# Kernel optimization log

Measured on AMD Instinct MI355X. Metric: run time of the kernel, lower is better.

Reference implementation:

```python
import jax, jax.numpy as jnp
import numpy as np

SAMPLE_RATE = 16000
N_TRANSIENTS = 20
TRANSIENT_SAMPLES = 1600  # int(0.1 s * 16000 Hz)
BATCH = 64
MAX_TRANSIENTS = 256
AUDIO_LEN = 160000  # 10 s @ 16 kHz


def setup_inputs() -> dict:
    key = jax.random.key(0)
    k1, k2, k3, k4 = jax.random.split(key, 4)
    # timings in seconds, sorted per batch (as in generate_random_transients)
    transient_timings = jnp.sort(
        jax.random.uniform(k1, (BATCH, MAX_TRANSIENTS), dtype=jnp.float32) * 9.0, axis=1)
    transient_ids = jax.random.randint(k2, (BATCH, MAX_TRANSIENTS), 0, N_TRANSIENTS)
    transient_gains = 0.1 + 0.9 * jax.random.uniform(k3, (BATCH, MAX_TRANSIENTS), dtype=jnp.float32)
    transient_templates = jax.random.normal(k4, (N_TRANSIENTS, TRANSIENT_SAMPLES), dtype=jnp.float32)
    return {
        "transient_timings": transient_timings,
        "transient_ids": transient_ids,
        "transient_gains": transient_gains,
        "transient_templates": transient_templates,
        "audio_length": AUDIO_LEN,
    }


def reference(transient_timings, transient_ids, transient_gains, transient_templates, audio_length):
    n_tr, L = transient_templates.shape
    # start sample of each transient (timings are non-negative, so floor == int())
    t_sample = jnp.floor(transient_timings * SAMPLE_RATE).astype(jnp.int32)  # [B, T]
    # skip conditions from the original loop: gain <= 0, id >= n_transients, start >= audio_length
    valid = (transient_gains > 0) & (transient_ids < n_tr) & (t_sample < audio_length)
    # gather templates: [B, T, L]
    tmpl = transient_templates[jnp.clip(transient_ids, 0, n_tr - 1)]
    vals = tmpl * (transient_gains * valid.astype(transient_gains.dtype))[..., None]
    # destination positions: [B, T, L]; positions >= audio_length are dropped (truncation)
    pos = t_sample[..., None] + jnp.arange(L, dtype=jnp.int32)

    def scatter_one(p, v):
        # p, v: [T, L] -> scatter-add into [audio_length]
        return jnp.zeros((audio_length,), v.dtype).at[p.reshape(-1)].add(
            v.reshape(-1), mode='drop')

    return jax.vmap(scatter_one)(pos, vals)  # [B, audio_length]
```

## Files before the change

kernel.cpp:

```cpp
#include <hip/hip_runtime.h>


constexpr int SR    = 16000;
constexpr int TL    = 1600;
constexpr int MAXT  = 256;
constexpr int NTHR  = 256;
constexpr int CHUNK = 1024;
constexpr int PAD   = 1024;
constexpr int ROWP  = PAD + TL + PAD;

__global__ __launch_bounds__(256)
void pad_templates(const float* __restrict__ templates, float* __restrict__ tpad, int n_tr)
{
    const int total = n_tr * ROWP;
    for (int i = blockIdx.x * blockDim.x + threadIdx.x; i < total;
         i += gridDim.x * blockDim.x) {
        const int r = i / ROWP;
        const int t = (i - r * ROWP) - PAD;
        tpad[i] = ((unsigned)t < (unsigned)TL) ? templates[r * TL + t] : 0.0f;
    }
}

__global__ __launch_bounds__(NTHR)
void transient_gather(const float* __restrict__ timings,
                      const int*   __restrict__ ids,
                      const float* __restrict__ gains,
                      const float* __restrict__ tpad,
                      float*       __restrict__ out,
                      int T, int n_tr, int A)
{
    __shared__ int2               s_m[MAXT];
    __shared__ unsigned long long s_mask[NTHR / 64];

    const int b      = blockIdx.y;
    const int chunk0 = blockIdx.x * CHUNK;
    const int tid    = (int)threadIdx.x;

    {
        const float tm = timings[(size_t)b * T + tid];
        const float g  = gains  [(size_t)b * T + tid];
        const int   id = ids    [(size_t)b * T + tid];
        const int   ts = (int)floorf(tm * (float)SR);
        const bool ok  = (g > 0.0f) & (id < n_tr) & (ts < A);
        const int tsc  = min(max(ts, 0), A);
        const int idc  = min(max(id, 0), n_tr - 1);
        s_m[tid] = make_int2((tsc << 8) | idc, ok ? __float_as_int(g) : 0);
        const bool ov = (tsc < chunk0 + CHUNK) && (tsc + TL > chunk0);
        const unsigned long long mball = __ballot(ov);
        if ((tid & 63) == 0) s_mask[tid >> 6] = mball;
    }
    __syncthreads();

    int lo = T, hi = -1;
#pragma unroll
    for (int w = 0; w < NTHR / 64; ++w) {
        const unsigned long long mw = s_mask[w];
        if (mw) {
            lo = min(lo, w * 64 + (int)__builtin_ctzll(mw));
            hi = max(hi, w * 64 + 63 - (int)__builtin_clzll(mw));
        }
    }

    float acc[4] = {0.f, 0.f, 0.f, 0.f};

    for (int j = lo; j <= hi; ++j) {
        const int2 mj = s_m[j];
        const int  mx  = __builtin_amdgcn_readfirstlane(mj.x);
        const int  mgb = __builtin_amdgcn_readfirstlane(mj.y);
        if (mgb == 0) continue;
        const float g  = __int_as_float(mgb);
        const int   ts = mx >> 8;
        const float* __restrict__ p =
            tpad + (size_t)(mx & 255) * ROWP + PAD + (chunk0 - ts);
#pragma unroll
        for (int k = 0; k < 4; ++k)
            acc[k] = fmaf(g, p[tid + k * NTHR], acc[k]);
    }

    float* ob = out + (size_t)b * A + chunk0 + tid;
#pragma unroll
    for (int k = 0; k < 4; ++k) {
        if (chunk0 + tid + k * NTHR < A)
            __builtin_nontemporal_store(acc[k], &ob[k * NTHR]);
    }
}

__global__ __launch_bounds__(NTHR)
void transient_gather_guard(const float* __restrict__ timings, const int* __restrict__ ids,
                            const float* __restrict__ gains, const float* __restrict__ templates,
                            float* __restrict__ out, int T, int n_tr, int A)
{
    __shared__ int2               s_m[MAXT];
    __shared__ unsigned long long s_mask[NTHR / 64];
    const int b = blockIdx.y, chunk0 = blockIdx.x * CHUNK, tid = (int)threadIdx.x;
    {
        const float tm = timings[(size_t)b * T + tid];
        const float g  = gains  [(size_t)b * T + tid];
        const int   id = ids    [(size_t)b * T + tid];
        const int   ts = (int)floorf(tm * (float)SR);
        const bool ok  = (g > 0.0f) & (id < n_tr) & (ts < A);
        const int tsc  = min(max(ts, 0), A);
        const int idc  = min(max(id, 0), n_tr - 1);
        s_m[tid] = make_int2((tsc << 8) | idc, ok ? __float_as_int(g) : 0);
        const bool ov = (tsc < chunk0 + CHUNK) && (tsc + TL > chunk0);
        const unsigned long long mball = __ballot(ov);
        if ((tid & 63) == 0) s_mask[tid >> 6] = mball;
    }
    __syncthreads();
    int lo = T, hi = -1;
#pragma unroll
    for (int w = 0; w < NTHR / 64; ++w) {
        const unsigned long long mw = s_mask[w];
        if (mw) {
            lo = min(lo, w * 64 + (int)__builtin_ctzll(mw));
            hi = max(hi, w * 64 + 63 - (int)__builtin_clzll(mw));
        }
    }
    float acc[4] = {0.f, 0.f, 0.f, 0.f};
    const int off_base = chunk0 + tid;
    for (int j = lo; j <= hi; ++j) {
        const int2 m = s_m[j];
        const int ts = m.x >> 8;
        const float g = __int_as_float(m.y);
        const float* __restrict__ row = templates + (size_t)(m.x & 255) * TL;
        const int off0 = off_base - ts;
#pragma unroll
        for (int k = 0; k < 4; ++k) {
            const int o = off0 + k * NTHR;
            if ((unsigned)o < (unsigned)TL) acc[k] += g * row[o];
        }
    }
    float* ob = out + (size_t)b * A + off_base;
#pragma unroll
    for (int k = 0; k < 4; ++k)
        if (off_base + k * NTHR < A) __builtin_nontemporal_store(acc[k], &ob[k * NTHR]);
}

extern "C" void kernel_launch(void* const* d_in, const int* in_sizes, int n_in,
                              void* d_out, int out_size, void* d_ws, size_t ws_size,
                              hipStream_t stream) {
    const float* timings   = (const float*)d_in[0];
    const int*   ids       = (const int*)  d_in[1];
    const float* gains     = (const float*)d_in[2];
    const float* templates = (const float*)d_in[3];
    float*       out       = (float*)d_out;

    const int T    = MAXT;
    const int B    = in_sizes[0] / T;
    const int n_tr = in_sizes[3] / TL;
    const int A    = out_size / B;

    dim3 grid((A + CHUNK - 1) / CHUNK, B), block(NTHR);
    const size_t need = (size_t)n_tr * ROWP * sizeof(float);
    if (ws_size >= need) {
        float* tpad = (float*)d_ws;
        pad_templates<<<dim3(80), dim3(256), 0, stream>>>(templates, tpad, n_tr);
        transient_gather<<<grid, block, 0, stream>>>(timings, ids, gains, tpad, out,
                                                     T, n_tr, A);
    } else {
        transient_gather_guard<<<grid, block, 0, stream>>>(timings, ids, gains, templates,
                                                           out, T, n_tr, A);
    }
}
```

Before: 25.06 us.

## Stage all templates in LDS and compute per-wave sub-chunks in one kernel

Replaces the pad-templates pre-kernel plus the global-memory gather with a single kernel that copies all 20 templates (128 KB) into shared memory. Each block handles a quarter of one batch row, and each wave processes 1024-sample sub-chunks with 16 accumulators per lane and per-wave ballot overlap detection. This removes the extra launch and the global or L2 template reads. In exchange it uses far fewer blocks (256 blocks of 1024 threads), each doing a large LDS fill per block, and adds clamped, predicated loads.

```diff
diff --git a/kernel.cpp b/kernel.cpp
--- a/kernel.cpp
+++ b/kernel.cpp
@@ -4,38 +4,114 @@
 constexpr int SR    = 16000;
 constexpr int TL    = 1600;
 constexpr int MAXT  = 256;
-constexpr int NTHR  = 256;
-constexpr int CHUNK = 1024;
-constexpr int PAD   = 1024;
-constexpr int ROWP  = PAD + TL + PAD;
+constexpr int NTR   = 20;
+constexpr int NTHR  = 1024;
+constexpr int SUB   = 1024;
+constexpr int KPL   = 16;
+constexpr int QUART = 4;
 
-__global__ __launch_bounds__(256)
-void pad_templates(const float* __restrict__ templates, float* __restrict__ tpad, int n_tr)
+__global__ __launch_bounds__(NTHR)
+void transient_lds(const float* __restrict__ timings,
+                   const int*   __restrict__ ids,
+                   const float* __restrict__ gains,
+                   const float* __restrict__ templates,
+                   float*       __restrict__ out,
+                   int T, int n_tr, int A)
 {
-    const int total = n_tr * ROWP;
-    for (int i = blockIdx.x * blockDim.x + threadIdx.x; i < total;
-         i += gridDim.x * blockDim.x) {
-        const int r = i / ROWP;
-        const int t = (i - r * ROWP) - PAD;
-        tpad[i] = ((unsigned)t < (unsigned)TL) ? templates[r * TL + t] : 0.0f;
+    __shared__ float s_tmpl[NTR * TL];
+    __shared__ int2  s_m[MAXT];
+
+    const int b    = blockIdx.x / QUART;
+    const int q    = blockIdx.x - b * QUART;
+    const int tid  = (int)threadIdx.x;
+    const int lane = tid & 63;
+    const int wave = tid >> 6;
+
+    const int qlen = (A + QUART - 1) / QUART;
+    const int q0   = q * qlen;
+    const int qend = min(A, q0 + qlen);
+
+    {
+        const float4* src = reinterpret_cast<const float4*>(templates);
+        float4*       dst = reinterpret_cast<float4*>(s_tmpl);
+        const int nv = (n_tr * TL) / 4;
+        for (int i = tid; i < nv; i += NTHR) dst[i] = src[i];
+    }
+    if (tid < T) {
+        const float tm = timings[(size_t)b * T + tid];
+        const float g  = gains  [(size_t)b * T + tid];
+        const int   id = ids    [(size_t)b * T + tid];
+        const int   ts = (int)floorf(tm * (float)SR);
+        const bool ok  = (g > 0.0f) & (id < n_tr) & (ts < A);
+        const int tsc  = min(max(ts, 0), A);
+        const int idc  = min(max(id, 0), n_tr - 1);
+        s_m[tid] = make_int2((tsc << 8) | idc, ok ? __float_as_int(g) : 0);
+    }
+    __syncthreads();
+
+    int tsr[4];
+#pragma unroll
+    for (int qq = 0; qq < 4; ++qq) tsr[qq] = s_m[qq * 64 + lane].x >> 8;
+
+    const int nsub = (qend - q0 + SUB - 1) / SUB;
+
+    for (int sc = wave; sc < nsub; sc += NTHR / 64) {
+        const int sub0 = q0 + sc * SUB;
+
+        int lo = T, hi = -1;
+#pragma unroll
+        for (int qq = 0; qq < 4; ++qq) {
+            const bool ov = (tsr[qq] < sub0 + SUB) & (tsr[qq] + TL > sub0);
+            const unsigned long long m = __ballot(ov);
+            if (m) {
+                lo = min(lo, qq * 64 + (int)__builtin_ctzll(m));
+                hi = max(hi, qq * 64 + 63 - (int)__builtin_clzll(m));
+            }
+        }
+
+        float acc[KPL];
+#pragma unroll
+        for (int k = 0; k < KPL; ++k) acc[k] = 0.0f;
+
+        for (int j = lo; j <= hi; ++j) {
+            const int2 mj  = s_m[j];
+            const int  mx  = __builtin_amdgcn_readfirstlane(mj.x);
+            const int  mgb = __builtin_amdgcn_readfirstlane(mj.y);
+            if (mgb == 0) continue;
+            const float g   = __int_as_float(mgb);
+            const int   ts  = mx >> 8;
+            const int   rb  = (mx & 255) * TL;
+            const int   dlt = sub0 - ts;
+#pragma unroll
+            for (int k = 0; k < KPL; ++k) {
+                const int offk = dlt + k * 64;
+                if (offk <= -64 || offk >= TL) continue;
+                const int o  = offk + lane;
+                const int oc = min(max(o, 0), TL - 1);
+                const float v = s_tmpl[rb + oc];
+                acc[k] = fmaf(((unsigned)o < (unsigned)TL) ? g : 0.0f, v, acc[k]);
+            }
+        }
+
+        float* ob = out + (size_t)b * A + sub0 + lane;
+#pragma unroll
+        for (int k = 0; k < KPL; ++k) {
+            if (sub0 + k * 64 + lane < qend)
+                __builtin_nontemporal_store(acc[k], &ob[k * 64]);
+        }
     }
 }
 
-__global__ __launch_bounds__(NTHR)
-void transient_gather(const float* __restrict__ timings,
-                      const int*   __restrict__ ids,
-                      const float* __restrict__ gains,
-                      const float* __restrict__ tpad,
-                      float*       __restrict__ out,
-                      int T, int n_tr, int A)
+constexpr int FNT   = 256;
+constexpr int FCH   = 1024;
+__global__ __launch_bounds__(FNT)
+void transient_gather_guard(const float* __restrict__ timings, const int* __restrict__ ids,
+                            const float* __restrict__ gains, const float* __restrict__ templates,
+                            float* __restrict__ out, int T, int n_tr, int A)
 {
     __shared__ int2               s_m[MAXT];
-    __shared__ unsigned long long s_mask[NTHR / 64];
-
-    const int b      = blockIdx.y;
-    const int chunk0 = blockIdx.x * CHUNK;
-    const int tid    = (int)threadIdx.x;
-
+    __shared__ unsigned long long s_mask[FNT / 64];
+    const int b = blockIdx.y, chunk0 = blockIdx.x * FCH, tid = (int)threadIdx.x;
     {
         const float tm = timings[(size_t)b * T + tid];
         const float g  = gains  [(size_t)b * T + tid];
@@ -45,71 +121,14 @@
         const int tsc  = min(max(ts, 0), A);
         const int idc  = min(max(id, 0), n_tr - 1);
         s_m[tid] = make_int2((tsc << 8) | idc, ok ? __float_as_int(g) : 0);
-        const bool ov = (tsc < chunk0 + CHUNK) && (tsc + TL > chunk0);
-        const unsigned long long mball = __ballot(ov);
-        if ((tid & 63) == 0) s_mask[tid >> 6] = mball;
-    }
-    __syncthreads();
-
-    int lo = T, hi = -1;
-#pragma unroll
-    for (int w = 0; w < NTHR / 64; ++w) {
-        const unsigned long long mw = s_mask[w];
-        if (mw) {
-            lo = min(lo, w * 64 + (int)__builtin_ctzll(mw));
-            hi = max(hi, w * 64 + 63 - (int)__builtin_clzll(mw));
-        }
-    }
-
-    float acc[4] = {0.f, 0.f, 0.f, 0.f};
-
-    for (int j = lo; j <= hi; ++j) {
-        const int2 mj = s_m[j];
-        const int  mx  = __builtin_amdgcn_readfirstlane(mj.x);
-        const int  mgb = __builtin_amdgcn_readfirstlane(mj.y);
-        if (mgb == 0) continue;
-        const float g  = __int_as_float(mgb);
-        const int   ts = mx >> 8;
-        const float* __restrict__ p =
-            tpad + (size_t)(mx & 255) * ROWP + PAD + (chunk0 - ts);
-#pragma unroll
-        for (int k = 0; k < 4; ++k)
-            acc[k] = fmaf(g, p[tid + k * NTHR], acc[k]);
-    }
-
-    float* ob = out + (size_t)b * A + chunk0 + tid;
-#pragma unroll
-    for (int k = 0; k < 4; ++k) {
-        if (chunk0 + tid + k * NTHR < A)
-            __builtin_nontemporal_store(acc[k], &ob[k * NTHR]);
-    }
-}
-
-__global__ __launch_bounds__(NTHR)
-void transient_gather_guard(const float* __restrict__ timings, const int* __restrict__ ids,
-                            const float* __restrict__ gains, const float* __restrict__ templates,
-                            float* __restrict__ out, int T, int n_tr, int A)
-{
-    __shared__ int2               s_m[MAXT];
-    __shared__ unsigned long long s_mask[NTHR / 64];
-    const int b = blockIdx.y, chunk0 = blockIdx.x * CHUNK, tid = (int)threadIdx.x;
-    {
-        const float tm = timings[(size_t)b * T + tid];
-        const float g  = gains  [(size_t)b * T + tid];
-        const int   id = ids    [(size_t)b * T + tid];
-        const int   ts = (int)floorf(tm * (float)SR);
-        const bool ok  = (g > 0.0f) & (id < n_tr) & (ts < A);
-        const int tsc  = min(max(ts, 0), A);
-        const int idc  = min(max(id, 0), n_tr - 1);
-        s_m[tid] = make_int2((tsc << 8) | idc, ok ? __float_as_int(g) : 0);
-        const bool ov = (tsc < chunk0 + CHUNK) && (tsc + TL > chunk0);
+        const bool ov = (tsc < chunk0 + FCH) && (tsc + TL > chunk0);
         const unsigned long long mball = __ballot(ov);
         if ((tid & 63) == 0) s_mask[tid >> 6] = mball;
     }
     __syncthreads();
     int lo = T, hi = -1;
 #pragma unroll
-    for (int w = 0; w < NTHR / 64; ++w) {
+    for (int w = 0; w < FNT / 64; ++w) {
         const unsigned long long mw = s_mask[w];
         if (mw) {
             lo = min(lo, w * 64 + (int)__builtin_ctzll(mw));
@@ -126,14 +145,14 @@
         const int off0 = off_base - ts;
 #pragma unroll
         for (int k = 0; k < 4; ++k) {
-            const int o = off0 + k * NTHR;
+            const int o = off0 + k * FNT;
             if ((unsigned)o < (unsigned)TL) acc[k] += g * row[o];
         }
     }
     float* ob = out + (size_t)b * A + off_base;
 #pragma unroll
     for (int k = 0; k < 4; ++k)
-        if (off_base + k * NTHR < A) __builtin_nontemporal_store(acc[k], &ob[k * NTHR]);
+        if (off_base + k * FNT < A) __builtin_nontemporal_store(acc[k], &ob[k * FNT]);
 }
 
 extern "C" void kernel_launch(void* const* d_in, const int* in_sizes, int n_in,
@@ -150,14 +169,12 @@
     const int n_tr = in_sizes[3] / TL;
     const int A    = out_size / B;
 
-    dim3 grid((A + CHUNK - 1) / CHUNK, B), block(NTHR);
-    const size_t need = (size_t)n_tr * ROWP * sizeof(float);
-    if (ws_size >= need) {
-        float* tpad = (float*)d_ws;
-        pad_templates<<<dim3(80), dim3(256), 0, stream>>>(templates, tpad, n_tr);
-        transient_gather<<<grid, block, 0, stream>>>(timings, ids, gains, tpad, out,
-                                                     T, n_tr, A);
+    if (n_tr <= NTR && (n_tr * TL) % 4 == 0) {
+        dim3 grid(B * QUART), block(NTHR);
+        transient_lds<<<grid, block, 0, stream>>>(timings, ids, gains, templates, out,
+                                                  T, n_tr, A);
     } else {
+        dim3 grid((A + FCH - 1) / FCH, B), block(FNT);
         transient_gather_guard<<<grid, block, 0, stream>>>(timings, ids, gains, templates,
                                                            out, T, n_tr, A);
     }
```

Measured after the change: 31.50 us. 25.7% more time.
